# Performance work log

Hardware: AMD Instinct MI355X
Metric: run time of the kernel (lower is better)

The kernel has to match this reference:

```python
import jax, jax.numpy as jnp
import numpy as np

NUM_HEADS = 12


def setup_inputs() -> dict:
    key = jax.random.key(0)
    ks = jax.random.split(key, 6)
    B, H, W, C = 8, 32, 32, 768
    hd = C // NUM_HEADS
    n = lambda k, shp, sc: jax.random.normal(k, shp, dtype=jnp.float32) * sc
    return {
        "x": n(ks[0], (B, H, W, C), 1.0),
        "qkv_w": n(ks[1], (3 * C, C), 0.02),
        "qkv_b": jnp.zeros((3 * C,), jnp.float32),
        "proj_w": n(ks[2], (C, C), 0.02),
        "proj_b": jnp.zeros((C,), jnp.float32),
        "rel_pos_h": n(ks[3], (2 * H - 1, hd), 0.02),
        "rel_pos_w": n(ks[4], (2 * W - 1, hd), 0.02),
    }


def reference(x, qkv_w, qkv_b, proj_w, proj_b, rel_pos_h, rel_pos_w):
    B, H, W, C = x.shape
    nH = NUM_HEADS
    hd = C // nH
    scale = hd ** -0.5
    # qkv projection (torch Linear convention: y = x @ W.T + b)
    qkv = x.reshape(B, H * W, C) @ qkv_w.T + qkv_b              # (B, HW, 3C)
    qkv = qkv.reshape(B, H * W, 3, nH, hd).transpose(2, 0, 3, 1, 4)
    qkv = qkv.reshape(3, B * nH, H * W, hd)
    q, k, v = qkv[0], qkv[1], qkv[2]
    attn = jnp.einsum('bqd,bkd->bqk', q * scale, k)             # (B*nH, HW, HW)
    # decomposed relative position bias (q_size == k_size, so no interpolation)
    coords_h = jnp.arange(H)[:, None] - jnp.arange(H)[None, :] + (H - 1)
    coords_w = jnp.arange(W)[:, None] - jnp.arange(W)[None, :] + (W - 1)
    Rh = rel_pos_h[coords_h]                                    # (H, H, hd)
    Rw = rel_pos_w[coords_w]                                    # (W, W, hd)
    r_q = q.reshape(B * nH, H, W, hd)
    rel_h = jnp.einsum('bhwc,hkc->bhwk', r_q, Rh)               # (B*nH, H, W, H)
    rel_w = jnp.einsum('bhwc,wkc->bhwk', r_q, Rw)               # (B*nH, H, W, W)
    attn = (attn.reshape(B * nH, H, W, H, W)
            + rel_h[..., :, None] + rel_w[..., None, :]).reshape(B * nH, H * W, H * W)
    attn = jax.nn.softmax(attn, axis=-1)
    out = attn @ v                                              # (B*nH, HW, hd)
    out = out.reshape(B, nH, H, W, hd).transpose(0, 2, 3, 1, 4).reshape(B, H, W, C)
    return out @ proj_w.T + proj_b
```

## Files before the change

### kernel.cpp

```cpp
#include <hip/hip_runtime.h>

using u16 = unsigned short;
using u32 = unsigned int;
typedef __attribute__((ext_vector_type(8))) short bf16x8;
typedef __attribute__((ext_vector_type(4))) float f32x4;

__device__ __forceinline__ float bf2f(u16 h) {
  union { u32 u; float f; } c; c.u = (u32)h << 16; return c.f;
}
__device__ __forceinline__ u16 f2bf(float f) {
  union { float f; u32 u; } c; c.f = f;
  u32 u = c.u;
  u32 r = (u + 0x7FFFu + ((u >> 16) & 1u)) >> 16;
  return (u16)r;
}

#define GLD16(gsrc, ldst)                                                      \
  __builtin_amdgcn_global_load_lds(                                            \
      (const __attribute__((address_space(1))) unsigned int*)(gsrc),           \
      (__attribute__((address_space(3))) unsigned int*)(ldst), 16, 0, 0)

__device__ __forceinline__ int kappa(int ss) {
  return (ss & 0x23) | ((ss & 0x10) >> 2) | ((ss & 0x0C) << 1);
}

__global__ void cvt_kernel(const float* __restrict__ src, u16* __restrict__ dst, int n) {
  int i = (blockIdx.x * blockDim.x + threadIdx.x) * 4;
  if (i < n) {
    float4 v = *(const float4*)(src + i);
    ushort4 o;
    o.x = f2bf(v.x); o.y = f2bf(v.y); o.z = f2bf(v.z); o.w = f2bf(v.w);
    *(ushort4*)(dst + i) = o;
  }
}

__global__ void tbl_kernel(const float* __restrict__ rph, const float* __restrict__ rpw,
                           u16* __restrict__ tbl) {
  int i = blockIdx.x * 256 + threadIdx.x;
  int row = i >> 6, d = i & 63;
  float v = 0.f;
  if (row < 63) v = rph[row * 64 + d];
  else if (row >= 64 && row < 127) v = rpw[(row - 64) * 64 + d];
  tbl[i] = f2bf(v * 1.44269504f);
}

__global__ __launch_bounds__(256, 2) void pgemm_kernel(
    const u16* __restrict__ A, const u16* __restrict__ tbl, u16* __restrict__ P) {
  __shared__ u16 As[128 * 64];
  __shared__ u16 Bs[128 * 64];
  const int tid = threadIdx.x;
  const int lane = tid & 63, wave = tid >> 6;
  const int lr = lane & 15, lg = lane >> 4;
  const int m0 = blockIdx.x * 128;
  const int wm = (wave >> 1) * 64, wn = (wave & 1) * 64;

#pragma unroll
  for (int i = 0; i < 4; ++i) {
    int c = tid + i * 256;
    int row = c >> 3, pp = c & 7;
    int pl = pp ^ (row & 7);
    GLD16(A + (size_t)(m0 + row) * 64 + pl * 8, &As[c * 8]);
    GLD16(tbl + row * 64 + pl * 8, &Bs[c * 8]);
  }
  __syncthreads();

  bf16x8 a[4][2], b[4][2];
#pragma unroll
  for (int m = 0; m < 4; ++m) {
    int row = wm + m * 16 + lr;
#pragma unroll
    for (int kf = 0; kf < 2; ++kf)
      a[m][kf] = *(const bf16x8*)&As[(row * 64 + kf * 32 + lg * 8) ^ ((row & 7) << 3)];
  }
#pragma unroll
  for (int n = 0; n < 4; ++n) {
    int row = wn + n * 16 + lr;
#pragma unroll
    for (int kf = 0; kf < 2; ++kf)
      b[n][kf] = *(const bf16x8*)&Bs[(row * 64 + kf * 32 + lg * 8) ^ ((row & 7) << 3)];
  }

  f32x4 acc[4][4] = {};
#pragma unroll
  for (int kf = 0; kf < 2; ++kf)
#pragma unroll
    for (int m = 0; m < 4; ++m)
#pragma unroll
      for (int n = 0; n < 4; ++n)
        acc[m][n] = __builtin_amdgcn_mfma_f32_16x16x32_bf16(a[m][kf], b[n][kf], acc[m][n], 0, 0, 0);

#pragma unroll
  for (int m = 0; m < 4; ++m)
#pragma unroll
    for (int n = 0; n < 4; ++n) {
      const int col = wn + n * 16 + lr;
#pragma unroll
      for (int r = 0; r < 4; ++r) {
        const int g = m0 + wm + m * 16 + lg * 4 + r;
        P[(size_t)g * 128 + col] = f2bf(acc[m][n][r]);
      }
    }
}

template <int MODE>
__global__ __launch_bounds__(512, 2) void gemm128(
    const u16* __restrict__ A, const u16* __restrict__ B,
    const float* __restrict__ bias, u16* __restrict__ oq, u16* __restrict__ ok,
    u16* __restrict__ ovt, float* __restrict__ ofp) {
  __shared__ u16 As[2][128 * 64];
  __shared__ u16 Bs[2][128 * 64];
  const int tid = threadIdx.x;
  const int lane = tid & 63, wave = tid >> 6;
  const int lr = lane & 15, lg = lane >> 4;

  const int nbx = (MODE == 0) ? 18 : 6;
  const int nwg = nbx * 64;
  int id = blockIdx.y * nbx + blockIdx.x;
  int nid = (id & 7) * (nwg >> 3) + (id >> 3);
  const int m0 = (nid / nbx) * 128, n0 = (nid % nbx) * 128;
  const int wm = (wave >> 2) * 64, wn = (wave & 3) * 32;

  f32x4 acc[4][2] = {};

  const u16* ap[2];
  const u16* bp[2];
#pragma unroll
  for (int i = 0; i < 2; ++i) {
    int c = tid + i * 512;
    int row = c >> 3, pp = c & 7;
    int pl = pp ^ (row & 7);
    if constexpr (MODE == 0) {
      ap[i] = A + (size_t)(m0 + row) * 768 + pl * 8;
    } else {
      int g = m0 + row;
      ap[i] = A + ((size_t)((g >> 10) * 12) << 16) + (g & 1023) * 64 + pl * 8;
    }
    bp[i] = B + (size_t)(n0 + row) * 768 + pl * 8;
  }
  constexpr int dA = (MODE == 0) ? 64 : 65536;

  auto stage = [&](int bi) {
#pragma unroll
    for (int i = 0; i < 2; ++i) {
      int c = tid + i * 512;
      GLD16(ap[i], &As[bi][c * 8]);
      GLD16(bp[i], &Bs[bi][c * 8]);
      ap[i] += dA;
      bp[i] += 64;
    }
  };

  stage(0);
#pragma unroll 1
  for (int t = 0; t < 12; ++t) {
    const int cur = t & 1;
    if (t < 11) {
      stage(cur ^ 1);
      asm volatile("s_waitcnt vmcnt(4)" ::: "memory");
    } else {
      asm volatile("s_waitcnt vmcnt(0)" ::: "memory");
    }
    __builtin_amdgcn_sched_barrier(0);
    __builtin_amdgcn_s_barrier();
    __builtin_amdgcn_sched_barrier(0);

    bf16x8 a[4][2], b[2][2];
#pragma unroll
    for (int m = 0; m < 4; ++m) {
      int row = wm + m * 16 + lr;
#pragma unroll
      for (int kf = 0; kf < 2; ++kf)
        a[m][kf] = *(const bf16x8*)&As[cur][(row * 64 + kf * 32 + lg * 8) ^ ((row & 7) << 3)];
    }
#pragma unroll
    for (int n = 0; n < 2; ++n) {
      int row = wn + n * 16 + lr;
#pragma unroll
      for (int kf = 0; kf < 2; ++kf)
        b[n][kf] = *(const bf16x8*)&Bs[cur][(row * 64 + kf * 32 + lg * 8) ^ ((row & 7) << 3)];
    }
    __builtin_amdgcn_s_setprio(1);
#pragma unroll
    for (int kf = 0; kf < 2; ++kf)
#pragma unroll
      for (int m = 0; m < 4; ++m)
#pragma unroll
        for (int n = 0; n < 2; ++n)
          acc[m][n] = __builtin_amdgcn_mfma_f32_16x16x32_bf16(a[m][kf], b[n][kf], acc[m][n], 0, 0, 0);
    __builtin_amdgcn_s_setprio(0);

    __builtin_amdgcn_sched_barrier(0);
    __builtin_amdgcn_s_barrier();
    __builtin_amdgcn_sched_barrier(0);
  }

#pragma unroll
  for (int m = 0; m < 4; ++m) {
    const int grow0 = m0 + wm + m * 16 + lg * 4;
#pragma unroll
    for (int n = 0; n < 2; ++n) {
      const int gcol = n0 + wn + n * 16 + lr;
      const float bv = bias[gcol];
      if constexpr (MODE == 0) {
        int which = (gcol >= 1536) ? 2 : (gcol >= 768 ? 1 : 0);
        int rem = gcol - which * 768;
        int bh = (grow0 >> 10) * 12 + (rem >> 6);
        if (which == 2) {
          int s0 = grow0 & 1023;
          int colb = (s0 & ~63) | kappa(s0 & 63);
          ushort4 pk;
          pk.x = f2bf(acc[m][n][0] + bv);
          pk.y = f2bf(acc[m][n][1] + bv);
          pk.z = f2bf(acc[m][n][2] + bv);
          pk.w = f2bf(acc[m][n][3] + bv);
          *(ushort4*)&ovt[((size_t)bh << 16) + (size_t)(rem & 63) * 1024 + colb] = pk;
        } else {
          u16* dst = (which == 0) ? oq : ok;
#pragma unroll
          for (int r = 0; r < 4; ++r) {
            int s = (grow0 & 1023) + r;
            dst[((size_t)bh << 16) + s * 64 + (rem & 63)] = f2bf(acc[m][n][r] + bv);
          }
        }
      } else {
#pragma unroll
        for (int r = 0; r < 4; ++r)
          ofp[(size_t)(grow0 + r) * 768 + gcol] = acc[m][n][r] + bv;
      }
    }
  }
}

__global__ __launch_bounds__(256, 4) void attn_kernel(
    const u16* __restrict__ qb, const u16* __restrict__ kb,
    const u16* __restrict__ vtb, const u16* __restrict__ pb,
    u16* __restrict__ ao) {
  __shared__ u16 Ks[2][64 * 64];
  __shared__ u16 Vs[2][64 * 64];

  const int tid = threadIdx.x;
  const int lane = tid & 63, wave = tid >> 6;
  const int lr = lane & 15, lg = lane >> 4;
  const int bh = blockIdx.x;
  const int q0 = blockIdx.y * 128 + wave * 32;
  const size_t hb = (size_t)bh << 16;

  bf16x8 qf[2][2];
#pragma unroll
  for (int m = 0; m < 2; ++m)
#pragma unroll
    for (int kf = 0; kf < 2; ++kf)
      qf[m][kf] = *(const bf16x8*)(qb + hb + (size_t)(q0 + m * 16 + lr) * 64 + kf * 32 + lg * 8);

  float rwv[2][2][4];
  const u16* bp[2];
#pragma unroll
  for (int m = 0; m < 2; ++m) {
    int g = q0 + m * 16 + lr;
    const size_t pbase = (((size_t)bh << 10) + g) * 128;
    int w = g & 31;
#pragma unroll
    for (int i = 0; i < 2; ++i)
#pragma unroll
      for (int r = 0; r < 4; ++r) {
        int kw = i * 16 + lg * 4 + r;
        rwv[m][i][r] = bf2f(pb[pbase + 95 + w - kw]);
      }
    bp[m] = pb + pbase + (g >> 5) + 31;
  }

  u16 bc0[2], bc1[2];
#pragma unroll
  for (int m = 0; m < 2; ++m) { bc0[m] = bp[m][0]; bc1[m] = bp[m][-1]; }

  float lsum[2] = {};
  f32x4 acco[2][4] = {};

  const u16* kp[2];
  const u16* vp[2];
#pragma unroll
  for (int i = 0; i < 2; ++i) {
    int c = tid + i * 256;
    int row = c >> 3, pp = c & 7;
    int pl = pp ^ (row & 7);
    kp[i] = kb + hb + (size_t)row * 64 + pl * 8;
    vp[i] = vtb + hb + (size_t)row * 1024 + pl * 8;
  }

  auto stage = [&](int bi) {
#pragma unroll
    for (int i = 0; i < 2; ++i) {
      int c = tid + i * 256;
      GLD16(kp[i], &Ks[bi][c * 8]);
      GLD16(vp[i], &Vs[bi][c * 8]);
      kp[i] += 4096;
      vp[i] += 64;
    }
  };

  stage(0);

  const float scale2 = 0.125f * 1.44269504f;

#pragma unroll 1
  for (int t = 0; t < 16; ++t) {
    const int cur = t & 1;
    u16 bn0[2], bn1[2];
    if (t < 15) {
      stage(cur ^ 1);
#pragma unroll
      for (int m = 0; m < 2; ++m) { bn0[m] = bp[m][-2]; bn1[m] = bp[m][-3]; }
      asm volatile("s_waitcnt vmcnt(8)" ::: "memory");
    } else {
      asm volatile("s_waitcnt vmcnt(0)" ::: "memory");
    }
    __builtin_amdgcn_sched_barrier(0);
    __builtin_amdgcn_s_barrier();
    __builtin_amdgcn_sched_barrier(0);

    f32x4 sac[2][4] = {};
    __builtin_amdgcn_s_setprio(1);
#pragma unroll
    for (int kf = 0; kf < 2; ++kf) {
#pragma unroll
      for (int f = 0; f < 4; ++f) {
        int row = f * 16 + lr;
        bf16x8 kv = *(const bf16x8*)&Ks[cur][(row * 64 + kf * 32 + lg * 8) ^ ((row & 7) << 3)];
#pragma unroll
        for (int m = 0; m < 2; ++m)
          sac[m][f] = __builtin_amdgcn_mfma_f32_16x16x32_bf16(kv, qf[m][kf], sac[m][f], 0, 0, 0);
      }
    }
    __builtin_amdgcn_s_setprio(0);

    bf16x8 paf[2][2];
#pragma unroll
    for (int m = 0; m < 2; ++m) {
      float c0 = bf2f(bc0[m]), c1 = bf2f(bc1[m]);
      float bs[2][2][4];
#pragma unroll
      for (int i = 0; i < 2; ++i)
#pragma unroll
        for (int r = 0; r < 4; ++r) {
          bs[0][i][r] = c0 + rwv[m][i][r];
          bs[1][i][r] = c1 + rwv[m][i][r];
        }
      union { u32 w[4]; bf16x8 v; } wa, wb;
#pragma unroll
      for (int f = 0; f < 4; ++f) {
        const int j = (f >> 1) & 1, i = f & 1;
        float p0 = __builtin_amdgcn_exp2f(sac[m][f][0] * scale2 + bs[j][i][0]);
        float p1 = __builtin_amdgcn_exp2f(sac[m][f][1] * scale2 + bs[j][i][1]);
        float p2 = __builtin_amdgcn_exp2f(sac[m][f][2] * scale2 + bs[j][i][2]);
        float p3 = __builtin_amdgcn_exp2f(sac[m][f][3] * scale2 + bs[j][i][3]);
        lsum[m] += (p0 + p1) + (p2 + p3);
        u32 w0, w1;
        asm("v_cvt_pk_bf16_f32 %0, %1, %2" : "=v"(w0) : "v"(p0), "v"(p1));
        asm("v_cvt_pk_bf16_f32 %0, %1, %2" : "=v"(w1) : "v"(p2), "v"(p3));
        if (f < 2) { wa.w[f * 2] = w0; wa.w[f * 2 + 1] = w1; }
        else       { wb.w[(f - 2) * 2] = w0; wb.w[(f - 2) * 2 + 1] = w1; }
      }
      paf[m][0] = wa.v;
      paf[m][1] = wb.v;
    }

    __builtin_amdgcn_s_setprio(1);
#pragma unroll
    for (int kf = 0; kf < 2; ++kf) {
#pragma unroll
      for (int fd = 0; fd < 4; ++fd) {
        int drow = fd * 16 + lr;
        bf16x8 vv = *(const bf16x8*)&Vs[cur][(drow * 64 + kf * 32 + lg * 8) ^ ((drow & 7) << 3)];
#pragma unroll
        for (int m = 0; m < 2; ++m)
          acco[m][fd] = __builtin_amdgcn_mfma_f32_16x16x32_bf16(paf[m][kf], vv, acco[m][fd], 0, 0, 0);
      }
    }
    __builtin_amdgcn_s_setprio(0);

    if (t < 15) {
#pragma unroll
      for (int m = 0; m < 2; ++m) {
        bc0[m] = bn0[m];
        bc1[m] = bn1[m];
        bp[m] -= 2;
      }
    }

    __builtin_amdgcn_sched_barrier(0);
    __builtin_amdgcn_s_barrier();
    __builtin_amdgcn_sched_barrier(0);
  }

#pragma unroll
  for (int m = 0; m < 2; ++m) {
    float s = lsum[m];
    s += __shfl_xor(s, 16);
    s += __shfl_xor(s, 32);
    float inv = 1.0f / s;
#pragma unroll
    for (int r = 0; r < 4; ++r) {
      int src = (lane & 48) + ((lane & 48) >> 2) + r;
      float invr = __shfl(inv, src);
      int gq = q0 + m * 16 + lg * 4 + r;
#pragma unroll
      for (int fd = 0; fd < 4; ++fd)
        ao[hb + (size_t)gq * 64 + fd * 16 + lr] = f2bf(acco[m][fd][r] * invr);
    }
  }
}

extern "C" void kernel_launch(void* const* d_in, const int* in_sizes, int n_in,
                              void* d_out, int out_size, void* d_ws, size_t ws_size,
                              hipStream_t stream) {
  const float* x = (const float*)d_in[0];
  const float* qkv_w = (const float*)d_in[1];
  const float* qkv_b = (const float*)d_in[2];
  const float* proj_w = (const float*)d_in[3];
  const float* proj_b = (const float*)d_in[4];
  const float* rel_pos_h = (const float*)d_in[5];
  const float* rel_pos_w = (const float*)d_in[6];
  float* out = (float*)d_out;

  char* ws = (char*)d_ws;
  u16* x_bf = (u16*)(ws + 0);
  u16* qkvw_bf = (u16*)(ws + 12582912);
  u16* projw_bf = (u16*)(ws + 16121856);
  u16* qbuf = (u16*)(ws + 17301504);
  u16* kbuf = (u16*)(ws + 29884416);
  u16* vtbuf = (u16*)(ws + 42467328);
  u16* pbuf = (u16*)(ws + 55050240);
  u16* tbl = (u16*)(ws + 80216064);
  u16* aobuf = x_bf;

  cvt_kernel<<<6144, 256, 0, stream>>>(x, x_bf, 6291456);
  cvt_kernel<<<1728, 256, 0, stream>>>(qkv_w, qkvw_bf, 1769472);
  cvt_kernel<<<576, 256, 0, stream>>>(proj_w, projw_bf, 589824);
  tbl_kernel<<<32, 256, 0, stream>>>(rel_pos_h, rel_pos_w, tbl);

  gemm128<0><<<dim3(18, 64), 512, 0, stream>>>(x_bf, qkvw_bf, qkv_b, qbuf, kbuf, vtbuf, nullptr);

  pgemm_kernel<<<768, 256, 0, stream>>>(qbuf, tbl, pbuf);

  attn_kernel<<<dim3(96, 8), 256, 0, stream>>>(qbuf, kbuf, vtbuf, pbuf, aobuf);

  gemm128<1><<<dim3(6, 64), 512, 0, stream>>>(aobuf, projw_bf, proj_b, nullptr, nullptr, nullptr, out);
}
```

Baseline: 145.6 us.

## Pre-gather rel-pos bias into compact per-query table held in registers

The relative-position projection kernel now writes the bias already indexed by key row/column into a compact 64-entry-per-query table, instead of the raw 128-wide diagonal layout. The attention kernel loads the 32 height-bias values once into registers with vector loads and shifts through them each iteration, which removes the scalar global loads inside the main loop and relaxes the vmcnt wait. Launch bounds drop from 4 to 2 blocks per SM to make room for the extra registers, which risks lower occupancy. The register shift loop (or its renaming after unroll) adds some per-iteration cost.

```diff
diff --git a/kernel.cpp b/kernel.cpp
--- a/kernel.cpp
+++ b/kernel.cpp
@@ -5,8 +5,8 @@
 typedef __attribute__((ext_vector_type(8))) short bf16x8;
 typedef __attribute__((ext_vector_type(4))) float f32x4;
 
-__device__ __forceinline__ float bf2f(u16 h) {
-  union { u32 u; float f; } c; c.u = (u32)h << 16; return c.f;
+__device__ __forceinline__ float bf2f(u32 h) {
+  union { u32 u; float f; } c; c.u = h << 16; return c.f;
 }
 __device__ __forceinline__ u16 f2bf(float f) {
   union { float f; u32 u; } c; c.f = f;
@@ -97,7 +97,16 @@
 #pragma unroll
       for (int r = 0; r < 4; ++r) {
         const int g = m0 + wm + m * 16 + lg * 4 + r;
-        P[(size_t)g * 128 + col] = f2bf(acc[m][n][r]);
+        const int s = g & 1023;
+        const int hq = s >> 5, w = s & 31;
+        u16 hv = f2bf(acc[m][n][r]);
+        if (col < 64) {
+          int kh = hq + 31 - col;
+          if ((unsigned)kh < 32u) P[(size_t)g * 64 + 32 + kh] = hv;
+        } else {
+          int kw = w + 95 - col;
+          if ((unsigned)kw < 32u) P[(size_t)g * 64 + kw] = hv;
+        }
       }
     }
 }
@@ -231,7 +240,7 @@
   }
 }
 
-__global__ __launch_bounds__(256, 4) void attn_kernel(
+__global__ __launch_bounds__(256, 2) void attn_kernel(
     const u16* __restrict__ qb, const u16* __restrict__ kb,
     const u16* __restrict__ vtb, const u16* __restrict__ pb,
     u16* __restrict__ ao) {
@@ -252,26 +261,25 @@
     for (int kf = 0; kf < 2; ++kf)
       qf[m][kf] = *(const bf16x8*)(qb + hb + (size_t)(q0 + m * 16 + lr) * 64 + kf * 32 + lg * 8);
 
+  u32 Wh[2][16];
   float rwv[2][2][4];
-  const u16* bp[2];
 #pragma unroll
   for (int m = 0; m < 2; ++m) {
     int g = q0 + m * 16 + lr;
-    const size_t pbase = (((size_t)bh << 10) + g) * 128;
-    int w = g & 31;
-#pragma unroll
-    for (int i = 0; i < 2; ++i)
-#pragma unroll
-      for (int r = 0; r < 4; ++r) {
-        int kw = i * 16 + lg * 4 + r;
-        rwv[m][i][r] = bf2f(pb[pbase + 95 + w - kw]);
-      }
-    bp[m] = pb + pbase + (g >> 5) + 31;
-  }
-
-  u16 bc0[2], bc1[2];
-#pragma unroll
-  for (int m = 0; m < 2; ++m) { bc0[m] = bp[m][0]; bc1[m] = bp[m][-1]; }
+    const u16* sb = pb + (((size_t)bh << 10) + g) * 64;
+    const uint4* s4 = (const uint4*)(sb + 32);
+    uint4 ha = s4[0], hc = s4[1], he = s4[2], hg = s4[3];
+    Wh[m][0] = ha.x;  Wh[m][1] = ha.y;  Wh[m][2] = ha.z;  Wh[m][3] = ha.w;
+    Wh[m][4] = hc.x;  Wh[m][5] = hc.y;  Wh[m][6] = hc.z;  Wh[m][7] = hc.w;
+    Wh[m][8] = he.x;  Wh[m][9] = he.y;  Wh[m][10] = he.z; Wh[m][11] = he.w;
+    Wh[m][12] = hg.x; Wh[m][13] = hg.y; Wh[m][14] = hg.z; Wh[m][15] = hg.w;
+    uint2 u0 = *(const uint2*)(sb + lg * 4);
+    uint2 u1 = *(const uint2*)(sb + 16 + lg * 4);
+    rwv[m][0][0] = bf2f(u0.x & 0xffffu); rwv[m][0][1] = bf2f(u0.x >> 16);
+    rwv[m][0][2] = bf2f(u0.y & 0xffffu); rwv[m][0][3] = bf2f(u0.y >> 16);
+    rwv[m][1][0] = bf2f(u1.x & 0xffffu); rwv[m][1][1] = bf2f(u1.x >> 16);
+    rwv[m][1][2] = bf2f(u1.y & 0xffffu); rwv[m][1][3] = bf2f(u1.y >> 16);
+  }
 
   float lsum[2] = {};
   f32x4 acco[2][4] = {};
@@ -305,12 +313,9 @@
 #pragma unroll 1
   for (int t = 0; t < 16; ++t) {
     const int cur = t & 1;
-    u16 bn0[2], bn1[2];
     if (t < 15) {
       stage(cur ^ 1);
-#pragma unroll
-      for (int m = 0; m < 2; ++m) { bn0[m] = bp[m][-2]; bn1[m] = bp[m][-3]; }
-      asm volatile("s_waitcnt vmcnt(8)" ::: "memory");
+      asm volatile("s_waitcnt vmcnt(4)" ::: "memory");
     } else {
       asm volatile("s_waitcnt vmcnt(0)" ::: "memory");
     }
@@ -336,7 +341,9 @@
     bf16x8 paf[2][2];
 #pragma unroll
     for (int m = 0; m < 2; ++m) {
-      float c0 = bf2f(bc0[m]), c1 = bf2f(bc1[m]);
+      u32 wrd = Wh[m][0];
+      float c0 = bf2f(wrd & 0xffffu);
+      float c1 = bf2f(wrd >> 16);
       float bs[2][2][4];
 #pragma unroll
       for (int i = 0; i < 2; ++i)
@@ -364,6 +371,9 @@
       paf[m][1] = wb.v;
     }
 
+#pragma unroll
+    for (int k = 0; k < 15; ++k) { Wh[0][k] = Wh[0][k + 1]; Wh[1][k] = Wh[1][k + 1]; }
+
     __builtin_amdgcn_s_setprio(1);
 #pragma unroll
     for (int kf = 0; kf < 2; ++kf) {
@@ -377,15 +387,6 @@
       }
     }
     __builtin_amdgcn_s_setprio(0);
-
-    if (t < 15) {
-#pragma unroll
-      for (int m = 0; m < 2; ++m) {
-        bc0[m] = bn0[m];
-        bc1[m] = bn1[m];
-        bp[m] -= 2;
-      }
-    }
 
     __builtin_amdgcn_sched_barrier(0);
     __builtin_amdgcn_s_barrier();
```

Measured after the change: 135.1 us. -7.2%, faster.
